# Kernel tuning notes

Measured on AMD Instinct MI355X. Metric: run time of the kernel, lower is better.

Reference implementation:

```python
import jax, jax.numpy as jnp
import numpy as np

N_COARSE = 64
N_FINE = 64  # n_fine_depth = 0
HIDDEN = 128
R = 16384


def setup_inputs() -> dict:
    key = jax.random.key(0)
    ks = jax.random.split(key, 8)
    origins = jax.random.normal(ks[0], (R, 3), dtype=jnp.float32)
    dirs = jax.random.normal(ks[1], (R, 3), dtype=jnp.float32)
    dirs = dirs / jnp.linalg.norm(dirs, axis=-1, keepdims=True)
    near = jnp.full((R, 1), 2.0, dtype=jnp.float32)
    far = jnp.full((R, 1), 6.0, dtype=jnp.float32)
    rays = jnp.concatenate([origins, dirs, near, far], axis=-1)  # [R, 8]
    u_coarse = jax.random.uniform(ks[2], (R, N_COARSE), dtype=jnp.float32)
    u_fine = jax.random.uniform(ks[3], (R, N_FINE), dtype=jnp.float32)
    u_jitter = jax.random.uniform(ks[4], (R, N_FINE), dtype=jnp.float32)
    W1 = jax.random.normal(ks[5], (3, HIDDEN), dtype=jnp.float32) * 0.5
    b1 = jnp.zeros((HIDDEN,), dtype=jnp.float32)
    W2 = jax.random.normal(ks[6], (HIDDEN, 4), dtype=jnp.float32) * 0.1
    b2 = jnp.zeros((4,), dtype=jnp.float32)
    return dict(rays=rays, u_coarse=u_coarse, u_fine=u_fine, u_jitter=u_jitter,
                W1=W1, b1=b1, W2=W2, b2=b2)


def _mlp(pts, W1, b1, W2, b2):
    # pts: [R, K, 3] -> [R, K, 4] (r, g, b, sigma)
    h = jax.nn.relu(pts @ W1 + b1)
    return h @ W2 + b2


def _composite(rays, z_sample, W1, b1, W2, b2):
    # z_sample: [R, K]; faithful to NeRFRenderer.composite
    deltas = jnp.concatenate(
        [z_sample[:, 1:] - z_sample[:, :-1], rays[:, 7:8] - z_sample[:, -1:]], axis=-1)
    pts = rays[:, None, :3] + z_sample[..., None] * rays[:, None, 3:6]  # [R, K, 3]
    out = _mlp(pts, W1, b1, W2, b2)
    rgbs = out[..., :3]
    sigmas = out[..., 3]
    alphas = 1.0 - jnp.exp(-deltas * jax.nn.relu(sigmas))
    alphas_shifted = jnp.concatenate(
        [jnp.ones_like(alphas[:, :1]), 1.0 - alphas + 1e-10], axis=-1)
    T = jnp.cumprod(alphas_shifted, axis=-1)
    weights = alphas * T[:, :-1]  # [R, K]
    rgb_final = jnp.sum(weights[..., None] * rgbs, axis=-2)  # [R, 3]
    depth_final = jnp.sum(weights * z_sample, axis=-1)       # [R]
    return weights, rgb_final, depth_final


def reference(rays, u_coarse, u_fine, u_jitter, W1, b1, W2, b2):
    near, far = rays[:, 6:7], rays[:, 7:8]
    # ---- coarse stratified sampling ----
    step = 1.0 / N_COARSE
    z_steps = jnp.linspace(0.0, 1.0 - step, N_COARSE, dtype=jnp.float32)[None, :] \
        + u_coarse * step
    z_coarse = near * (1.0 - z_steps) + far * z_steps  # [R, Kc] (lindisp=False)
    w_c, rgb_c, depth_c = _composite(rays, z_coarse, W1, b1, W2, b2)
    # ---- fine importance sampling (inverse CDF on detached coarse weights) ----
    w = jax.lax.stop_gradient(w_c) + 1e-5
    pdf = w / jnp.sum(w, axis=-1, keepdims=True)
    cdf = jnp.cumsum(pdf, axis=-1)
    cdf = jnp.concatenate([jnp.zeros_like(cdf[:, :1]), cdf], axis=-1)  # [R, Kc+1]
    inds = jax.vmap(lambda c, u: jnp.searchsorted(c, u, side='right'))(cdf, u_fine)
    inds = jnp.maximum(inds.astype(jnp.float32) - 1.0, 0.0)
    zf_steps = (inds + u_jitter) / N_COARSE
    z_fine = near * (1.0 - zf_steps) + far * zf_steps  # [R, Kf]
    z_all = jnp.sort(jnp.concatenate([z_coarse, z_fine], axis=-1), axis=-1)  # [R, Kc+Kf]
    w_f, rgb_f, depth_f = _composite(rays, z_all, W1, b1, W2, b2)
    # pack outputs: [R, 8] = [coarse rgb(3), coarse depth(1), fine rgb(3), fine depth(1)]
    return jnp.concatenate(
        [rgb_c, depth_c[:, None], rgb_f, depth_f[:, None]], axis=-1)
```

## Files before the change

### kernel.cpp

```cpp
#include <hip/hip_runtime.h>

#define HID 128

typedef _Float16 f16x8 __attribute__((ext_vector_type(8)));
typedef _Float16 f16x2 __attribute__((ext_vector_type(2)));
typedef float f32x4 __attribute__((ext_vector_type(4)));

union HV { f16x8 v; f16x2 h[4]; };

__device__ __forceinline__ float wshfl(float v, int src)   { return __shfl(v, src, 64); }
__device__ __forceinline__ float wshfl_up(float v, int d)  { return __shfl_up(v, d, 64); }
__device__ __forceinline__ float wshfl_dn(float v, int d)  { return __shfl_down(v, d, 64); }
__device__ __forceinline__ float wshfl_xor(float v, int m) { return __shfl_xor(v, m, 64); }

__device__ __forceinline__ float wave_sum(float v) {
#pragma unroll
    for (int m = 32; m >= 1; m >>= 1) v += wshfl_xor(v, m);
    return v;
}

__device__ __forceinline__ float wave_iscan_add(float v, int lane) {
#pragma unroll
    for (int d = 1; d < 64; d <<= 1) {
        float t = wshfl_up(v, d);
        if (lane >= d) v += t;
    }
    return v;
}

__device__ __forceinline__ float wave_iscan_mul(float v, int lane) {
#pragma unroll
    for (int d = 1; d < 64; d <<= 1) {
        float t = wshfl_up(v, d);
        if (lane >= d) v *= t;
    }
    return v;
}

__device__ __forceinline__ f32x4 mlp_tile(float x, float y, float z,
                                          const _Float16* __restrict__ wls,
                                          const f16x8* __restrict__ w2t,
                                          f32x4 cini, int g) {
    const _Float16 xs = (_Float16)x, ys = (_Float16)y, zs = (_Float16)z;
    const f16x2 xp = { xs, xs };
    const f16x2 yp = { ys, ys };
    const f16x2 zp = { zs, zs };
    const f16x2 zero2 = { (_Float16)0, (_Float16)0 };
    f32x4 C = cini;
#pragma unroll
    for (int c = 0; c < 4; ++c) {
        const int hid0 = 32 * c + 8 * g;
        HV w0 = *(const HV*)&wls[hid0];
        HV w1 = *(const HV*)&wls[HID + hid0];
        HV w2 = *(const HV*)&wls[2 * HID + hid0];
        HV bb = *(const HV*)&wls[3 * HID + hid0];
        HV hb;
#pragma unroll
        for (int r = 0; r < 4; ++r) {
            f16x2 acc = w0.h[r] * xp + bb.h[r];
            acc = w1.h[r] * yp + acc;
            acc = w2.h[r] * zp + acc;
            hb.h[r] = __builtin_elementwise_max(acc, zero2);
        }
        C = __builtin_amdgcn_mfma_f32_16x16x32_f16(w2t[c], hb.v, C, 0, 0, 0);
    }
    return C;
}

extern "C" __global__ void __launch_bounds__(256)
nerf_fused(const float* __restrict__ rays,
           const float* __restrict__ u_coarse,
           const float* __restrict__ u_fine,
           const float* __restrict__ u_jitter,
           const float* __restrict__ W1,
           const float* __restrict__ b1,
           const float* __restrict__ W2,
           const float* __restrict__ b2,
           float* __restrict__ out) {
    const int lane = threadIdx.x & 63;
    const int wv   = threadIdx.x >> 6;
    const int ray  = (blockIdx.x << 2) + wv;
    const int s16  = lane & 15;
    const int g    = lane >> 4;

    __shared__ _Float16 wls[4 * HID];
    __shared__ float s_cdf [4][65];
    __shared__ float s_zc  [4][64];
    __shared__ float s_zf  [4][64];
    __shared__ float s_za  [4][130];
    __shared__ float s_rgba[4][128][4];

    {
        const int tid = threadIdx.x;
        if (tid < 192) {
            f16x2 p = { (_Float16)W1[2 * tid], (_Float16)W1[2 * tid + 1] };
            *(f16x2*)&wls[2 * tid] = p;
        } else {
            const int i = tid - 192;
            f16x2 p = { (_Float16)b1[2 * i], (_Float16)b1[2 * i + 1] };
            *(f16x2*)&wls[384 + 2 * i] = p;
        }
    }
    __syncthreads();

    f16x8 w2t[4];
#pragma unroll
    for (int c = 0; c < 4; ++c) {
        HV u;
#pragma unroll
        for (int r = 0; r < 4; ++r) {
            const int k0 = 32 * c + 8 * g + 2 * r;
            float a0 = 0.0f, a1 = 0.0f;
            if (s16 < 4) {
                a0 = W2[k0 * 4 + s16];
                a1 = W2[(k0 + 1) * 4 + s16];
            }
            f16x2 p = { (_Float16)a0, (_Float16)a1 };
            u.h[r] = p;
        }
        w2t[c] = u.v;
    }
    f32x4 cini;
    {
        const float c0 = b2[0], c1 = b2[1], c2 = b2[2], c3 = b2[3];
        cini[0] = (g == 0) ? c0 : 0.0f;
        cini[1] = (g == 0) ? c1 : 0.0f;
        cini[2] = (g == 0) ? c2 : 0.0f;
        cini[3] = (g == 0) ? c3 : 0.0f;
    }

    const float* rp = rays + ray * 8;
    const float ox = rp[0], oy = rp[1], oz = rp[2];
    const float dx = rp[3], dy = rp[4], dz = rp[5];
    const float nearv = rp[6], farv = rp[7];

    const float uc = u_coarse[(ray << 6) + lane];
    const float zsv = ((float)lane + uc) * 0.015625f;
    const float zc = nearv * (1.0f - zsv) + farv * zsv;
    s_zc[wv][lane] = zc;

#pragma unroll
    for (int t = 0; t < 4; ++t) {
        const float zt = s_zc[wv][t * 16 + s16];
        f32x4 C = mlp_tile(fmaf(zt, dx, ox), fmaf(zt, dy, oy), fmaf(zt, dz, oz),
                           wls, w2t, cini, g);
        if (lane < 16) {
            *(float4*)&s_rgba[wv][t * 16 + s16][0] = make_float4(C[0], C[1], C[2], C[3]);
        }
    }

    {
        const float4 cv = *(const float4*)&s_rgba[wv][lane][0];
        const float znext = wshfl_dn(zc, 1);
        const float delta = (lane == 63) ? (farv - zc) : (znext - zc);
        const float alpha = 1.0f - __expf(-delta * fmaxf(cv.w, 0.0f));

        float f  = 1.0f - alpha + 1e-10f;
        float ip = wave_iscan_mul(f, lane);
        float Te = wshfl_up(ip, 1);
        if (lane == 0) Te = 1.0f;
        const float w = alpha * Te;

        const float rc = wave_sum(w * cv.x);
        const float gc = wave_sum(w * cv.y);
        const float bc = wave_sum(w * cv.z);
        const float dc = wave_sum(w * zc);

        float wp = w + 1e-5f;
        float cs = wave_iscan_add(wp, lane);
        float total = wshfl(cs, 63);
        if (lane == 0) s_cdf[wv][0] = 0.0f;
        s_cdf[wv][lane + 1] = cs / total;

        if (lane == 0) {
            float4* op = (float4*)(out + ray * 8);
            op[0] = make_float4(rc, gc, bc, dc);
        }
    }

    const float uf = u_fine[(ray << 6) + lane];
    const float uj = u_jitter[(ray << 6) + lane];

    int lo = 0, hi = 65;
#pragma unroll
    for (int it = 0; it < 7; ++it) {
        if (lo < hi) {
            int mid = (lo + hi) >> 1;
            if (s_cdf[wv][mid] <= uf) lo = mid + 1; else hi = mid;
        }
    }
    const float ind = fmaxf((float)lo - 1.0f, 0.0f);
    const float zfs = (ind + uj) * 0.015625f;
    const float zfv = nearv * (1.0f - zfs) + farv * zfs;

    float v = zfv;
#pragma unroll
    for (int k = 2; k <= 64; k <<= 1) {
#pragma unroll
        for (int j = k >> 1; j > 0; j >>= 1) {
            float other = wshfl_xor(v, j);
            bool asc = ((lane & k) == 0);
            bool low = ((lane & j) == 0);
            float mn = fminf(v, other), mx = fmaxf(v, other);
            v = (asc == low) ? mn : mx;
        }
    }
    s_zf[wv][lane] = v;

    int lof = 0, hif = 64;
#pragma unroll
    for (int it = 0; it < 7; ++it) {
        if (lof < hif) {
            int mid = (lof + hif) >> 1;
            if (s_zf[wv][mid] < zc) lof = mid + 1; else hif = mid;
        }
    }
    int loc = 0, hic = 64;
#pragma unroll
    for (int it = 0; it < 7; ++it) {
        if (loc < hic) {
            int mid = (loc + hic) >> 1;
            if (s_zc[wv][mid] <= v) loc = mid + 1; else hic = mid;
        }
    }
    s_za[wv][lane + lof] = zc;
    s_za[wv][lane + loc] = v;

#pragma unroll
    for (int t = 0; t < 8; ++t) {
        const float zt = s_za[wv][t * 16 + s16];
        f32x4 C = mlp_tile(fmaf(zt, dx, ox), fmaf(zt, dy, oy), fmaf(zt, dz, oz),
                           wls, w2t, cini, g);
        if (lane < 16) {
            *(float4*)&s_rgba[wv][t * 16 + s16][0] = make_float4(C[0], C[1], C[2], C[3]);
        }
    }

    {
        const float z0 = s_za[wv][2 * lane];
        const float z1 = s_za[wv][2 * lane + 1];
        const float z2 = (lane == 63) ? farv : s_za[wv][2 * lane + 2];
        const float4 v0 = *(const float4*)&s_rgba[wv][2 * lane][0];
        const float4 v1 = *(const float4*)&s_rgba[wv][2 * lane + 1][0];

        const float d0 = z1 - z0;
        const float d1 = z2 - z1;
        const float a0 = 1.0f - __expf(-d0 * fmaxf(v0.w, 0.0f));
        const float a1 = 1.0f - __expf(-d1 * fmaxf(v1.w, 0.0f));
        const float f0 = 1.0f - a0 + 1e-10f;
        const float f1 = 1.0f - a1 + 1e-10f;

        float pl = f0 * f1;
        float ip = wave_iscan_mul(pl, lane);
        float Ee = wshfl_up(ip, 1);
        if (lane == 0) Ee = 1.0f;

        const float w0 = a0 * Ee;
        const float w1 = a1 * Ee * f0;

        const float rf = wave_sum(fmaf(w0, v0.x, w1 * v1.x));
        const float gf = wave_sum(fmaf(w0, v0.y, w1 * v1.y));
        const float bf = wave_sum(fmaf(w0, v0.z, w1 * v1.z));
        const float df = wave_sum(fmaf(w0, z0, w1 * z1));

        if (lane == 0) {
            float4* op = (float4*)(out + ray * 8);
            op[1] = make_float4(rf, gf, bf, df);
        }
    }
}

extern "C" void kernel_launch(void* const* d_in, const int* in_sizes, int n_in,
                              void* d_out, int out_size, void* d_ws, size_t ws_size,
                              hipStream_t stream) {
    const float* rays = (const float*)d_in[0];
    const float* uc   = (const float*)d_in[1];
    const float* uf   = (const float*)d_in[2];
    const float* uj   = (const float*)d_in[3];
    const float* W1   = (const float*)d_in[4];
    const float* b1   = (const float*)d_in[5];
    const float* W2   = (const float*)d_in[6];
    const float* b2   = (const float*)d_in[7];
    float* o          = (float*)d_out;

    const int R = in_sizes[0] / 8;
    dim3 grid(R / 4), block(256);
    hipLaunchKernelGGL(nerf_fused, grid, block, 0, stream,
                       rays, uc, uf, uj, W1, b1, W2, b2, o);
}
```

Baseline: 128.8 us.

## Keep MLP weights and MFMA outputs in registers, drop LDS staging

Each lane now loads and converts W1/b1 straight into registers, which removes the shared weight table and the block barrier. MFMA results are no longer written to LDS and read back. Every lane replicates W2 and b2 across all output rows and groups, then picks its own tile's result with selects. The fine composite is reorganised into two 64-sample halves with two scans and a carried transmittance product, which matches the new lane mapping. This raises register pressure and adds redundant MFMA output work in exchange for less LDS traffic and synchronisation.

```diff
diff --git a/kernel.cpp b/kernel.cpp
--- a/kernel.cpp
+++ b/kernel.cpp
@@ -37,29 +37,42 @@
     return v;
 }
 
+__device__ __forceinline__ HV cvt8(const float* __restrict__ p) {
+    const float4 lo = *(const float4*)p;
+    const float4 hi = *(const float4*)(p + 4);
+    HV u;
+    u.h[0] = f16x2{ (_Float16)lo.x, (_Float16)lo.y };
+    u.h[1] = f16x2{ (_Float16)lo.z, (_Float16)lo.w };
+    u.h[2] = f16x2{ (_Float16)hi.x, (_Float16)hi.y };
+    u.h[3] = f16x2{ (_Float16)hi.z, (_Float16)hi.w };
+    return u;
+}
+
+__device__ __forceinline__ f32x4 selg(f32x4 a, f32x4 b, f32x4 c, f32x4 d, int g) {
+    f32x4 r = a;
+    r = (g == 1) ? b : r;
+    r = (g == 2) ? c : r;
+    r = (g == 3) ? d : r;
+    return r;
+}
+
 __device__ __forceinline__ f32x4 mlp_tile(float x, float y, float z,
-                                          const _Float16* __restrict__ wls,
-                                          const f16x8* __restrict__ w2t,
-                                          f32x4 cini, int g) {
+                                          const HV rw0[4], const HV rw1[4],
+                                          const HV rw2[4], const HV rb[4],
+                                          const f16x8 w2t[4], f32x4 C) {
     const _Float16 xs = (_Float16)x, ys = (_Float16)y, zs = (_Float16)z;
     const f16x2 xp = { xs, xs };
     const f16x2 yp = { ys, ys };
     const f16x2 zp = { zs, zs };
     const f16x2 zero2 = { (_Float16)0, (_Float16)0 };
-    f32x4 C = cini;
 #pragma unroll
     for (int c = 0; c < 4; ++c) {
-        const int hid0 = 32 * c + 8 * g;
-        HV w0 = *(const HV*)&wls[hid0];
-        HV w1 = *(const HV*)&wls[HID + hid0];
-        HV w2 = *(const HV*)&wls[2 * HID + hid0];
-        HV bb = *(const HV*)&wls[3 * HID + hid0];
         HV hb;
 #pragma unroll
         for (int r = 0; r < 4; ++r) {
-            f16x2 acc = w0.h[r] * xp + bb.h[r];
-            acc = w1.h[r] * yp + acc;
-            acc = w2.h[r] * zp + acc;
+            f16x2 acc = rw0[c].h[r] * xp + rb[c].h[r];
+            acc = rw1[c].h[r] * yp + acc;
+            acc = rw2[c].h[r] * zp + acc;
             hb.h[r] = __builtin_elementwise_max(acc, zero2);
         }
         C = __builtin_amdgcn_mfma_f32_16x16x32_f16(w2t[c], hb.v, C, 0, 0, 0);
@@ -83,26 +96,20 @@
     const int s16  = lane & 15;
     const int g    = lane >> 4;
 
-    __shared__ _Float16 wls[4 * HID];
-    __shared__ float s_cdf [4][65];
-    __shared__ float s_zc  [4][64];
-    __shared__ float s_zf  [4][64];
-    __shared__ float s_za  [4][130];
-    __shared__ float s_rgba[4][128][4];
-
-    {
-        const int tid = threadIdx.x;
-        if (tid < 192) {
-            f16x2 p = { (_Float16)W1[2 * tid], (_Float16)W1[2 * tid + 1] };
-            *(f16x2*)&wls[2 * tid] = p;
-        } else {
-            const int i = tid - 192;
-            f16x2 p = { (_Float16)b1[2 * i], (_Float16)b1[2 * i + 1] };
-            *(f16x2*)&wls[384 + 2 * i] = p;
-        }
-    }
-    __syncthreads();
-
+    __shared__ float s_cdf[4][65];
+    __shared__ float s_zc [4][64];
+    __shared__ float s_zf [4][64];
+    __shared__ float s_za [4][130];
+
+    HV rw0[4], rw1[4], rw2[4], rb[4];
+#pragma unroll
+    for (int c = 0; c < 4; ++c) {
+        const int hid0 = 32 * c + 8 * g;
+        rw0[c] = cvt8(W1 + hid0);
+        rw1[c] = cvt8(W1 + HID + hid0);
+        rw2[c] = cvt8(W1 + 2 * HID + hid0);
+        rb [c] = cvt8(b1 + hid0);
+    }
     f16x8 w2t[4];
 #pragma unroll
     for (int c = 0; c < 4; ++c) {
@@ -110,24 +117,14 @@
 #pragma unroll
         for (int r = 0; r < 4; ++r) {
             const int k0 = 32 * c + 8 * g + 2 * r;
-            float a0 = 0.0f, a1 = 0.0f;
-            if (s16 < 4) {
-                a0 = W2[k0 * 4 + s16];
-                a1 = W2[(k0 + 1) * 4 + s16];
-            }
-            f16x2 p = { (_Float16)a0, (_Float16)a1 };
-            u.h[r] = p;
+            const float a0 = W2[k0 * 4 + (s16 & 3)];
+            const float a1 = W2[(k0 + 1) * 4 + (s16 & 3)];
+            u.h[r] = f16x2{ (_Float16)a0, (_Float16)a1 };
         }
         w2t[c] = u.v;
     }
     f32x4 cini;
-    {
-        const float c0 = b2[0], c1 = b2[1], c2 = b2[2], c3 = b2[3];
-        cini[0] = (g == 0) ? c0 : 0.0f;
-        cini[1] = (g == 0) ? c1 : 0.0f;
-        cini[2] = (g == 0) ? c2 : 0.0f;
-        cini[3] = (g == 0) ? c3 : 0.0f;
-    }
+    cini[0] = b2[0]; cini[1] = b2[1]; cini[2] = b2[2]; cini[3] = b2[3];
 
     const float* rp = rays + ray * 8;
     const float ox = rp[0], oy = rp[1], oz = rp[2];
@@ -139,21 +136,22 @@
     const float zc = nearv * (1.0f - zsv) + farv * zsv;
     s_zc[wv][lane] = zc;
 
-#pragma unroll
-    for (int t = 0; t < 4; ++t) {
-        const float zt = s_zc[wv][t * 16 + s16];
-        f32x4 C = mlp_tile(fmaf(zt, dx, ox), fmaf(zt, dy, oy), fmaf(zt, dz, oz),
-                           wls, w2t, cini, g);
-        if (lane < 16) {
-            *(float4*)&s_rgba[wv][t * 16 + s16][0] = make_float4(C[0], C[1], C[2], C[3]);
-        }
-    }
-
-    {
-        const float4 cv = *(const float4*)&s_rgba[wv][lane][0];
+    float zt[4];
+#pragma unroll
+    for (int t = 0; t < 4; ++t) zt[t] = s_zc[wv][t * 16 + s16];
+    f32x4 C0, C1, C2, C3;
+    {
+        C0 = mlp_tile(fmaf(zt[0], dx, ox), fmaf(zt[0], dy, oy), fmaf(zt[0], dz, oz), rw0, rw1, rw2, rb, w2t, cini);
+        C1 = mlp_tile(fmaf(zt[1], dx, ox), fmaf(zt[1], dy, oy), fmaf(zt[1], dz, oz), rw0, rw1, rw2, rb, w2t, cini);
+        C2 = mlp_tile(fmaf(zt[2], dx, ox), fmaf(zt[2], dy, oy), fmaf(zt[2], dz, oz), rw0, rw1, rw2, rb, w2t, cini);
+        C3 = mlp_tile(fmaf(zt[3], dx, ox), fmaf(zt[3], dy, oy), fmaf(zt[3], dz, oz), rw0, rw1, rw2, rb, w2t, cini);
+    }
+    const f32x4 cv = selg(C0, C1, C2, C3, g);
+
+    {
         const float znext = wshfl_dn(zc, 1);
         const float delta = (lane == 63) ? (farv - zc) : (znext - zc);
-        const float alpha = 1.0f - __expf(-delta * fmaxf(cv.w, 0.0f));
+        const float alpha = 1.0f - __expf(-delta * fmaxf(cv[3], 0.0f));
 
         float f  = 1.0f - alpha + 1e-10f;
         float ip = wave_iscan_mul(f, lane);
@@ -161,9 +159,9 @@
         if (lane == 0) Te = 1.0f;
         const float w = alpha * Te;
 
-        const float rc = wave_sum(w * cv.x);
-        const float gc = wave_sum(w * cv.y);
-        const float bc = wave_sum(w * cv.z);
+        const float rc = wave_sum(w * cv[0]);
+        const float gc = wave_sum(w * cv[1]);
+        const float bc = wave_sum(w * cv[2]);
         const float dc = wave_sum(w * zc);
 
         float wp = w + 1e-5f;
@@ -226,42 +224,56 @@
     s_za[wv][lane + lof] = zc;
     s_za[wv][lane + loc] = v;
 
-#pragma unroll
-    for (int t = 0; t < 8; ++t) {
-        const float zt = s_za[wv][t * 16 + s16];
-        f32x4 C = mlp_tile(fmaf(zt, dx, ox), fmaf(zt, dy, oy), fmaf(zt, dz, oz),
-                           wls, w2t, cini, g);
-        if (lane < 16) {
-            *(float4*)&s_rgba[wv][t * 16 + s16][0] = make_float4(C[0], C[1], C[2], C[3]);
-        }
-    }
-
-    {
-        const float z0 = s_za[wv][2 * lane];
-        const float z1 = s_za[wv][2 * lane + 1];
-        const float z2 = (lane == 63) ? farv : s_za[wv][2 * lane + 2];
-        const float4 v0 = *(const float4*)&s_rgba[wv][2 * lane][0];
-        const float4 v1 = *(const float4*)&s_rgba[wv][2 * lane + 1][0];
-
-        const float d0 = z1 - z0;
-        const float d1 = z2 - z1;
-        const float a0 = 1.0f - __expf(-d0 * fmaxf(v0.w, 0.0f));
-        const float a1 = 1.0f - __expf(-d1 * fmaxf(v1.w, 0.0f));
-        const float f0 = 1.0f - a0 + 1e-10f;
-        const float f1 = 1.0f - a1 + 1e-10f;
-
-        float pl = f0 * f1;
-        float ip = wave_iscan_mul(pl, lane);
-        float Ee = wshfl_up(ip, 1);
-        if (lane == 0) Ee = 1.0f;
-
-        const float w0 = a0 * Ee;
-        const float w1 = a1 * Ee * f0;
-
-        const float rf = wave_sum(fmaf(w0, v0.x, w1 * v1.x));
-        const float gf = wave_sum(fmaf(w0, v0.y, w1 * v1.y));
-        const float bf = wave_sum(fmaf(w0, v0.z, w1 * v1.z));
-        const float df = wave_sum(fmaf(w0, z0, w1 * z1));
+    float zu[8];
+#pragma unroll
+    for (int t = 0; t < 8; ++t) zu[t] = s_za[wv][t * 16 + s16];
+
+    f32x4 vA, vB;
+    {
+        f32x4 F0 = mlp_tile(fmaf(zu[0], dx, ox), fmaf(zu[0], dy, oy), fmaf(zu[0], dz, oz), rw0, rw1, rw2, rb, w2t, cini);
+        f32x4 F1 = mlp_tile(fmaf(zu[1], dx, ox), fmaf(zu[1], dy, oy), fmaf(zu[1], dz, oz), rw0, rw1, rw2, rb, w2t, cini);
+        f32x4 F2 = mlp_tile(fmaf(zu[2], dx, ox), fmaf(zu[2], dy, oy), fmaf(zu[2], dz, oz), rw0, rw1, rw2, rb, w2t, cini);
+        f32x4 F3 = mlp_tile(fmaf(zu[3], dx, ox), fmaf(zu[3], dy, oy), fmaf(zu[3], dz, oz), rw0, rw1, rw2, rb, w2t, cini);
+        vA = selg(F0, F1, F2, F3, g);
+    }
+    {
+        f32x4 F4 = mlp_tile(fmaf(zu[4], dx, ox), fmaf(zu[4], dy, oy), fmaf(zu[4], dz, oz), rw0, rw1, rw2, rb, w2t, cini);
+        f32x4 F5 = mlp_tile(fmaf(zu[5], dx, ox), fmaf(zu[5], dy, oy), fmaf(zu[5], dz, oz), rw0, rw1, rw2, rb, w2t, cini);
+        f32x4 F6 = mlp_tile(fmaf(zu[6], dx, ox), fmaf(zu[6], dy, oy), fmaf(zu[6], dz, oz), rw0, rw1, rw2, rb, w2t, cini);
+        f32x4 F7 = mlp_tile(fmaf(zu[7], dx, ox), fmaf(zu[7], dy, oy), fmaf(zu[7], dz, oz), rw0, rw1, rw2, rb, w2t, cini);
+        vB = selg(F4, F5, F6, F7, g);
+    }
+
+    {
+        const float zA = s_za[wv][lane];
+        const float zB = s_za[wv][lane + 64];
+
+        const float zA1 = wshfl_dn(zA, 1);
+        const float zB0 = wshfl(zB, 0);
+        const float zB1 = wshfl_dn(zB, 1);
+        const float dA = (lane == 63) ? (zB0 - zA) : (zA1 - zA);
+        const float dB = (lane == 63) ? (farv - zB) : (zB1 - zB);
+
+        const float aA = 1.0f - __expf(-dA * fmaxf(vA[3], 0.0f));
+        const float aB = 1.0f - __expf(-dB * fmaxf(vB[3], 0.0f));
+        const float fA = 1.0f - aA + 1e-10f;
+        const float fB = 1.0f - aB + 1e-10f;
+
+        float ipA = wave_iscan_mul(fA, lane);
+        float TA  = wshfl_up(ipA, 1);
+        if (lane == 0) TA = 1.0f;
+        const float wA = aA * TA;
+
+        const float Pall = wshfl(ipA, 63);
+        float ipB = wave_iscan_mul(fB, lane);
+        float TBp = wshfl_up(ipB, 1);
+        if (lane == 0) TBp = 1.0f;
+        const float wB = aB * Pall * TBp;
+
+        const float rf = wave_sum(fmaf(wA, vA[0], wB * vB[0]));
+        const float gf = wave_sum(fmaf(wA, vA[1], wB * vB[1]));
+        const float bf = wave_sum(fmaf(wA, vA[2], wB * vB[2]));
+        const float df = wave_sum(fmaf(wA, zA, wB * zB));
 
         if (lane == 0) {
             float4* op = (float4*)(out + ray * 8);
```

New measurement: 129.0 us. No clear change (+0.2%).
